# Kernel optimization log

Measured on AMD Instinct MI355X. Metric: run time of the kernel, lower is better.

## Reference

```python
import jax, jax.numpy as jnp
import numpy as np

STATE_DIM = 4        # per-block state size (rel pos + rel vel, 2D)
N_NEIGH = 64         # neighbors per agent
BATCH = 4096         # observations in the batch (len(x) in torch code)
PHI_H, PHI_OUT = 256, 64
RHO_H, ACTION_DIM = 256, 2
R_AGENT = 0.15
A_MAX = 2.0


def setup_inputs() -> dict:
    key = jax.random.key(0)
    ks = jax.random.split(key, 5)

    def w(k, i, o):
        return jax.random.normal(k, (i, o), jnp.float32) / np.sqrt(i).astype(np.float32)

    x = jax.random.normal(ks[0], (BATCH, (N_NEIGH + 2) * STATE_DIM), jnp.float32)
    return dict(
        x=x,
        phi_w1=w(ks[1], STATE_DIM, PHI_H), phi_b1=jnp.zeros((PHI_H,), jnp.float32),
        phi_w2=w(ks[2], PHI_H, PHI_OUT), phi_b2=jnp.zeros((PHI_OUT,), jnp.float32),
        rho_w1=w(ks[3], PHI_OUT, RHO_H), rho_b1=jnp.zeros((RHO_H,), jnp.float32),
        rho_w2=w(ks[4], RHO_H, ACTION_DIM), rho_b2=jnp.zeros((ACTION_DIM,), jnp.float32),
    )


def reference(x, phi_w1, phi_b1, phi_w2, phi_b2, rho_w1, rho_b1, rho_w2, rho_b2):
    B = x.shape[0]
    blocks = x.reshape(B, -1, STATE_DIM)                 # [B, n_n+2, sd]
    # DeepSet: phi per block, permutation-invariant sum, rho head.
    h = jax.nn.relu(jnp.einsum('bns,sh->bnh', blocks, phi_w1) + phi_b1)
    phi = jnp.einsum('bnh,ho->bno', h, phi_w2) + phi_b2  # [B, n_n+2, phi_out]
    X = phi.sum(axis=1)                                  # [B, phi_out]
    h2 = jax.nn.relu(X @ rho_w1 + rho_b1)
    a = A_MAX * jnp.tanh(h2 @ rho_w2 + rho_b2)           # [B, action_dim]
    # Barrier: neighbor blocks start at block index 2; take first half (positions).
    p = blocks[:, 2:, : STATE_DIM // 2]                  # [B, n_n, 2]
    d = jnp.linalg.norm(p, axis=-1, keepdims=True)       # [B, n_n, 1]
    barrier = jnp.sum(-p / (d - R_AGENT) ** 2, axis=1)   # [B, 2]
    barrier = jax.lax.stop_gradient(barrier)  # torch goes through numpy -> detached
    a = a + barrier
    scale = A_MAX / jnp.max(a)  # torch.max(a_max)/torch.max(a_wbarrier), global max
    return jnp.where(scale < 1.0, a * scale, a)
```

## Files before the change

### kernel.cpp

```cpp
#include <hip/hip_runtime.h>
#include <math.h>


#define GROWS 4
#define NBLOCKS (4096 / GROWS)

__device__ __forceinline__ unsigned fkey(float f) {
    unsigned u = __float_as_uint(f);
    return (u & 0x80000000u) ? ~u : (u | 0x80000000u);
}
__device__ __forceinline__ float fkey_inv(unsigned k) {
    return __uint_as_float((k & 0x80000000u) ? (k & 0x7fffffffu) : ~k);
}
__device__ __forceinline__ float rlane(float v, int i) {
    return __uint_as_float(__builtin_amdgcn_readlane(__float_as_uint(v), i));
}

__global__ __launch_bounds__(256, 4) void barrier_net_main(
    const float* __restrict__ x,
    const float* __restrict__ w1,  const float* __restrict__ b1,
    const float* __restrict__ w2,  const float* __restrict__ b2,
    const float* __restrict__ rw1, const float* __restrict__ rb1,
    const float* __restrict__ rw2, const float* __restrict__ rb2,
    float* __restrict__ out, unsigned* __restrict__ maxkey)
{
    __shared__ float sH[GROWS][264];
    __shared__ float sXp[4][GROWS][68];
    __shared__ float sP4[4][GROWS][2];
    __shared__ float sbar[GROWS][2];
    __shared__ float sa[GROWS * 2];

    const int tid = threadIdx.x;
    const int ln  = tid & 63;
    const int wv  = tid >> 6;
    const int b0  = blockIdx.x * GROWS;
    const int row = b0 + wv;
    const float4* __restrict__ x4 = (const float4*)(x + (size_t)row * 264);

    float4 xr = x4[ln];
    float4 pv = x4[ln + 2];

    float4 w1r0 = ((const float4*)(w1      ))[ln];
    float4 w1r1 = ((const float4*)(w1 + 256))[ln];
    float4 w1r2 = ((const float4*)(w1 + 512))[ln];
    float4 w1r3 = ((const float4*)(w1 + 768))[ln];
    float4 b1r  = ((const float4*)b1)[ln];
    float a0 = 0.f, a1 = 0.f, a2 = 0.f, a3 = 0.f;
    #define P1_STEP(X0, X1, X2, X3)                                        \
    do {                                                                   \
        float h0 = b1r.x, h1 = b1r.y, h2 = b1r.z, h3 = b1r.w;              \
        h0 = fmaf(X0, w1r0.x, h0); h1 = fmaf(X0, w1r0.y, h1);              \
        h2 = fmaf(X0, w1r0.z, h2); h3 = fmaf(X0, w1r0.w, h3);              \
        h0 = fmaf(X1, w1r1.x, h0); h1 = fmaf(X1, w1r1.y, h1);              \
        h2 = fmaf(X1, w1r1.z, h2); h3 = fmaf(X1, w1r1.w, h3);              \
        h0 = fmaf(X2, w1r2.x, h0); h1 = fmaf(X2, w1r2.y, h1);              \
        h2 = fmaf(X2, w1r2.z, h2); h3 = fmaf(X2, w1r2.w, h3);              \
        h0 = fmaf(X3, w1r3.x, h0); h1 = fmaf(X3, w1r3.y, h1);              \
        h2 = fmaf(X3, w1r3.z, h2); h3 = fmaf(X3, w1r3.w, h3);              \
        a0 += fmaxf(h0, 0.f); a1 += fmaxf(h1, 0.f);                        \
        a2 += fmaxf(h2, 0.f); a3 += fmaxf(h3, 0.f);                        \
    } while (0)

    #pragma unroll 8
    for (int n = 0; n < 64; n++) {
        float X0 = rlane(xr.x, n), X1 = rlane(xr.y, n),
              X2 = rlane(xr.z, n), X3 = rlane(xr.w, n);
        P1_STEP(X0, X1, X2, X3);
    }
    {
        float X0 = rlane(pv.x, 62), X1 = rlane(pv.y, 62),
              X2 = rlane(pv.z, 62), X3 = rlane(pv.w, 62);
        P1_STEP(X0, X1, X2, X3);
        X0 = rlane(pv.x, 63); X1 = rlane(pv.y, 63);
        X2 = rlane(pv.z, 63); X3 = rlane(pv.w, 63);
        P1_STEP(X0, X1, X2, X3);
    }
    ((float4*)sH[wv])[ln] = make_float4(a0, a1, a2, a3);

    {
        float px = pv.x, py = pv.y;
        float d  = sqrtf(px * px + py * py);
        float t  = d - 0.15f;
        float inv = 1.0f / (t * t);
        float bx = -px * inv, by = -py * inv;
        #pragma unroll
        for (int m = 32; m >= 1; m >>= 1) {
            bx += __shfl_xor(bx, m);
            by += __shfl_xor(by, m);
        }
        if (ln == 0) { sbar[wv][0] = bx; sbar[wv][1] = by; }
    }
    __syncthreads();

    float Hq0 = sH[0][(wv << 6) + ln];
    float Hq1 = sH[1][(wv << 6) + ln];
    float Hq2 = sH[2][(wv << 6) + ln];
    float Hq3 = sH[3][(wv << 6) + ln];
    {
        float xp0 = 0.f, xp1 = 0.f, xp2 = 0.f, xp3 = 0.f;
        const float* w2q = w2 + (wv << 12);
        #pragma unroll 16
        for (int i = 0; i < 64; i++) {
            float wv2 = w2q[(i << 6) + ln];
            xp0 = fmaf(rlane(Hq0, i), wv2, xp0);
            xp1 = fmaf(rlane(Hq1, i), wv2, xp1);
            xp2 = fmaf(rlane(Hq2, i), wv2, xp2);
            xp3 = fmaf(rlane(Hq3, i), wv2, xp3);
        }
        sXp[wv][0][ln] = xp0; sXp[wv][1][ln] = xp1;
        sXp[wv][2][ln] = xp2; sXp[wv][3][ln] = xp3;
    }
    __syncthreads();

    float bb = 66.0f * b2[ln];
    float Xf0 = sXp[0][0][ln] + sXp[1][0][ln] + sXp[2][0][ln] + sXp[3][0][ln] + bb;
    float Xf1 = sXp[0][1][ln] + sXp[1][1][ln] + sXp[2][1][ln] + sXp[3][1][ln] + bb;
    float Xf2 = sXp[0][2][ln] + sXp[1][2][ln] + sXp[2][2][ln] + sXp[3][2][ln] + bb;
    float Xf3 = sXp[0][3][ln] + sXp[1][3][ln] + sXp[2][3][ln] + sXp[3][3][ln] + bb;

    float c0, c1, c2, c3;
    c0 = c1 = c2 = c3 = rb1[tid];
    #pragma unroll 16
    for (int i = 0; i < 64; i++) {
        float rwv = rw1[(i << 8) + tid];
        c0 = fmaf(rlane(Xf0, i), rwv, c0);
        c1 = fmaf(rlane(Xf1, i), rwv, c1);
        c2 = fmaf(rlane(Xf2, i), rwv, c2);
        c3 = fmaf(rlane(Xf3, i), rwv, c3);
    }
    c0 = fmaxf(c0, 0.f); c1 = fmaxf(c1, 0.f);
    c2 = fmaxf(c2, 0.f); c3 = fmaxf(c3, 0.f);

    {
        float2 r2 = ((const float2*)rw2)[tid];
        float p00 = c0 * r2.x, p01 = c0 * r2.y;
        float p10 = c1 * r2.x, p11 = c1 * r2.y;
        float p20 = c2 * r2.x, p21 = c2 * r2.y;
        float p30 = c3 * r2.x, p31 = c3 * r2.y;
        #pragma unroll
        for (int m = 32; m >= 1; m >>= 1) {
            p00 += __shfl_xor(p00, m); p01 += __shfl_xor(p01, m);
            p10 += __shfl_xor(p10, m); p11 += __shfl_xor(p11, m);
            p20 += __shfl_xor(p20, m); p21 += __shfl_xor(p21, m);
            p30 += __shfl_xor(p30, m); p31 += __shfl_xor(p31, m);
        }
        if (ln == 0) {
            sP4[wv][0][0] = p00; sP4[wv][0][1] = p01;
            sP4[wv][1][0] = p10; sP4[wv][1][1] = p11;
            sP4[wv][2][0] = p20; sP4[wv][2][1] = p21;
            sP4[wv][3][0] = p30; sP4[wv][3][1] = p31;
        }
    }
    __syncthreads();

    if (tid < GROWS * 2) {
        int r = tid >> 1, c = tid & 1;
        float pre = sP4[0][r][c] + sP4[1][r][c] + sP4[2][r][c] + sP4[3][r][c] + rb2[c];
        float a = 2.0f * tanhf(pre) + sbar[r][c];
        out[(b0 + r) * 2 + c] = a;
        sa[tid] = a;
    }
    __syncthreads();
    if (tid == 0) {
        float m = sa[0];
        #pragma unroll
        for (int i = 1; i < GROWS * 2; i++) m = fmaxf(m, sa[i]);
        atomicMax(maxkey, fkey(m));
    }
}

__global__ __launch_bounds__(256) void barrier_net_scale(
    float* __restrict__ out, const unsigned* __restrict__ maxkey)
{
    int i = blockIdx.x * 256 + threadIdx.x;
    float amax  = fkey_inv(*maxkey);
    float scale = 2.0f / amax;
    float a = out[i];
    out[i] = (scale < 1.0f) ? a * scale : a;
}

extern "C" void kernel_launch(void* const* d_in, const int* in_sizes, int n_in,
                              void* d_out, int out_size, void* d_ws, size_t ws_size,
                              hipStream_t stream) {
    const float* x   = (const float*)d_in[0];
    const float* w1  = (const float*)d_in[1];
    const float* b1  = (const float*)d_in[2];
    const float* w2  = (const float*)d_in[3];
    const float* b2  = (const float*)d_in[4];
    const float* rw1 = (const float*)d_in[5];
    const float* rb1 = (const float*)d_in[6];
    const float* rw2 = (const float*)d_in[7];
    const float* rb2 = (const float*)d_in[8];
    float* out = (float*)d_out;
    unsigned* maxkey = (unsigned*)d_ws;

    hipMemsetAsync(d_ws, 0, 4, stream);
    barrier_net_main<<<NBLOCKS, 256, 0, stream>>>(
        x, w1, b1, w2, b2, rw1, rb1, rw2, rb2, out, maxkey);
    barrier_net_scale<<<8192 / 256, 256, 0, stream>>>(out, maxkey);
}
```

Baseline: 102.3 us.

## Fuse global-max rescale into main kernel via last-block counter; fully unroll readlane loops

Drops the separate rescale kernel. Each block bumps an atomic counter after its atomicMax, and the last block to finish reads the global max and rescales all 8192 outputs itself. All three readlane loops are also fully unrolled so the lane indices become compile-time immediates. This removes one kernel launch and its gap, but puts a serial 8192-element rescale on a single block at the tail and adds code size and register pressure from the full unrolling.

```diff
diff --git a/kernel.cpp b/kernel.cpp
--- a/kernel.cpp
+++ b/kernel.cpp
@@ -12,23 +12,24 @@
 __device__ __forceinline__ float fkey_inv(unsigned k) {
     return __uint_as_float((k & 0x80000000u) ? (k & 0x7fffffffu) : ~k);
 }
-__device__ __forceinline__ float rlane(float v, int i) {
+__device__ __forceinline__ float rlane_imm(float v, int i) {
     return __uint_as_float(__builtin_amdgcn_readlane(__float_as_uint(v), i));
 }
 
-__global__ __launch_bounds__(256, 4) void barrier_net_main(
+__global__ __launch_bounds__(256, 4) void barrier_net_fused(
     const float* __restrict__ x,
     const float* __restrict__ w1,  const float* __restrict__ b1,
     const float* __restrict__ w2,  const float* __restrict__ b2,
     const float* __restrict__ rw1, const float* __restrict__ rb1,
     const float* __restrict__ rw2, const float* __restrict__ rb2,
-    float* __restrict__ out, unsigned* __restrict__ maxkey)
+    float* __restrict__ out, unsigned* __restrict__ ws)
 {
     __shared__ float sH[GROWS][264];
     __shared__ float sXp[4][GROWS][68];
     __shared__ float sP4[4][GROWS][2];
     __shared__ float sbar[GROWS][2];
     __shared__ float sa[GROWS * 2];
+    __shared__ int   sLast;
 
     const int tid = threadIdx.x;
     const int ln  = tid & 63;
@@ -61,18 +62,18 @@
         a2 += fmaxf(h2, 0.f); a3 += fmaxf(h3, 0.f);                        \
     } while (0)
 
-    #pragma unroll 8
+    #pragma unroll
     for (int n = 0; n < 64; n++) {
-        float X0 = rlane(xr.x, n), X1 = rlane(xr.y, n),
-              X2 = rlane(xr.z, n), X3 = rlane(xr.w, n);
+        float X0 = rlane_imm(xr.x, n), X1 = rlane_imm(xr.y, n),
+              X2 = rlane_imm(xr.z, n), X3 = rlane_imm(xr.w, n);
         P1_STEP(X0, X1, X2, X3);
     }
     {
-        float X0 = rlane(pv.x, 62), X1 = rlane(pv.y, 62),
-              X2 = rlane(pv.z, 62), X3 = rlane(pv.w, 62);
+        float X0 = rlane_imm(pv.x, 62), X1 = rlane_imm(pv.y, 62),
+              X2 = rlane_imm(pv.z, 62), X3 = rlane_imm(pv.w, 62);
         P1_STEP(X0, X1, X2, X3);
-        X0 = rlane(pv.x, 63); X1 = rlane(pv.y, 63);
-        X2 = rlane(pv.z, 63); X3 = rlane(pv.w, 63);
+        X0 = rlane_imm(pv.x, 63); X1 = rlane_imm(pv.y, 63);
+        X2 = rlane_imm(pv.z, 63); X3 = rlane_imm(pv.w, 63);
         P1_STEP(X0, X1, X2, X3);
     }
     ((float4*)sH[wv])[ln] = make_float4(a0, a1, a2, a3);
@@ -99,13 +100,13 @@
     {
         float xp0 = 0.f, xp1 = 0.f, xp2 = 0.f, xp3 = 0.f;
         const float* w2q = w2 + (wv << 12);
-        #pragma unroll 16
+        #pragma unroll
         for (int i = 0; i < 64; i++) {
             float wv2 = w2q[(i << 6) + ln];
-            xp0 = fmaf(rlane(Hq0, i), wv2, xp0);
-            xp1 = fmaf(rlane(Hq1, i), wv2, xp1);
-            xp2 = fmaf(rlane(Hq2, i), wv2, xp2);
-            xp3 = fmaf(rlane(Hq3, i), wv2, xp3);
+            xp0 = fmaf(rlane_imm(Hq0, i), wv2, xp0);
+            xp1 = fmaf(rlane_imm(Hq1, i), wv2, xp1);
+            xp2 = fmaf(rlane_imm(Hq2, i), wv2, xp2);
+            xp3 = fmaf(rlane_imm(Hq3, i), wv2, xp3);
         }
         sXp[wv][0][ln] = xp0; sXp[wv][1][ln] = xp1;
         sXp[wv][2][ln] = xp2; sXp[wv][3][ln] = xp3;
@@ -120,13 +121,13 @@
 
     float c0, c1, c2, c3;
     c0 = c1 = c2 = c3 = rb1[tid];
-    #pragma unroll 16
+    #pragma unroll
     for (int i = 0; i < 64; i++) {
         float rwv = rw1[(i << 8) + tid];
-        c0 = fmaf(rlane(Xf0, i), rwv, c0);
-        c1 = fmaf(rlane(Xf1, i), rwv, c1);
-        c2 = fmaf(rlane(Xf2, i), rwv, c2);
-        c3 = fmaf(rlane(Xf3, i), rwv, c3);
+        c0 = fmaf(rlane_imm(Xf0, i), rwv, c0);
+        c1 = fmaf(rlane_imm(Xf1, i), rwv, c1);
+        c2 = fmaf(rlane_imm(Xf2, i), rwv, c2);
+        c3 = fmaf(rlane_imm(Xf3, i), rwv, c3);
     }
     c0 = fmaxf(c0, 0.f); c1 = fmaxf(c1, 0.f);
     c2 = fmaxf(c2, 0.f); c3 = fmaxf(c3, 0.f);
@@ -161,22 +162,30 @@
         sa[tid] = a;
     }
     __syncthreads();
+
     if (tid == 0) {
         float m = sa[0];
         #pragma unroll
         for (int i = 1; i < GROWS * 2; i++) m = fmaxf(m, sa[i]);
-        atomicMax(maxkey, fkey(m));
-    }
-}
-
-__global__ __launch_bounds__(256) void barrier_net_scale(
-    float* __restrict__ out, const unsigned* __restrict__ maxkey)
-{
-    int i = blockIdx.x * 256 + threadIdx.x;
-    float amax  = fkey_inv(*maxkey);
-    float scale = 2.0f / amax;
-    float a = out[i];
-    out[i] = (scale < 1.0f) ? a * scale : a;
+        atomicMax(&ws[0], fkey(m));
+        __threadfence();
+        unsigned old = atomicAdd(&ws[1], 1u);
+        sLast = (old == NBLOCKS - 1u);
+    }
+    __syncthreads();
+
+    if (sLast) {
+        __threadfence();
+        unsigned k = atomicMax(&ws[0], 0u);
+        float scale = 2.0f / fkey_inv(k);
+        if (scale < 1.0f) {
+            for (int i = tid; i < 4096 * 2; i += 256) {
+                float a = __hip_atomic_load(&out[i], __ATOMIC_RELAXED,
+                                            __HIP_MEMORY_SCOPE_AGENT);
+                out[i] = a * scale;
+            }
+        }
+    }
 }
 
 extern "C" void kernel_launch(void* const* d_in, const int* in_sizes, int n_in,
@@ -192,10 +201,9 @@
     const float* rw2 = (const float*)d_in[7];
     const float* rb2 = (const float*)d_in[8];
     float* out = (float*)d_out;
-    unsigned* maxkey = (unsigned*)d_ws;
-
-    hipMemsetAsync(d_ws, 0, 4, stream);
-    barrier_net_main<<<NBLOCKS, 256, 0, stream>>>(
-        x, w1, b1, w2, b2, rw1, rb1, rw2, rb2, out, maxkey);
-    barrier_net_scale<<<8192 / 256, 256, 0, stream>>>(out, maxkey);
-}
+    unsigned* ws = (unsigned*)d_ws;
+
+    hipMemsetAsync(d_ws, 0, 8, stream);
+    barrier_net_fused<<<NBLOCKS, 256, 0, stream>>>(
+        x, w1, b1, w2, b2, rw1, rb1, rw2, rb2, out, ws);
+}
```

New measurement: 115.9 us. 13.3% more time.
